# Optimization experiments

Hardware: AMD Instinct MI355X
Metric: run time of the kernel (lower is better)

Reference implementation:

```python
import jax, jax.numpy as jnp
import numpy as np

N, E = 50000, 800000
IN_C, HID, OUT_C = 128, 64, 40

def setup_inputs() -> dict:
    key = jax.random.key(0)
    ks = jax.random.split(key, 16)
    def w(k, shape, fan_in):
        return jax.random.normal(k, shape, dtype=jnp.float32) * (1.0 / np.sqrt(fan_in))
    x = jax.random.normal(ks[0], (N, IN_C), dtype=jnp.float32)
    edge_index = jax.random.randint(ks[1], (2, E), 0, N, dtype=jnp.int64)
    return {
        "x": x,
        "edge_index": edge_index,
        "W1": w(ks[2], (IN_C, HID), IN_C), "b1": jnp.zeros((HID,), jnp.float32),
        "W2": w(ks[3], (HID, HID), HID),   "b2": jnp.zeros((HID,), jnp.float32),
        "W3": w(ks[4], (HID, HID), HID),   "b3": jnp.zeros((HID,), jnp.float32),
        "g1": jnp.ones((HID,), jnp.float32), "be1": jnp.zeros((HID,), jnp.float32),
        "g2": jnp.ones((HID,), jnp.float32), "be2": jnp.zeros((HID,), jnp.float32),
        "M1": w(ks[5], (HID, HID), HID),   "mb1": jnp.zeros((HID,), jnp.float32),
        "M2": w(ks[6], (HID, OUT_C), HID), "mb2": jnp.zeros((OUT_C,), jnp.float32),
        "batch_size": N,
    }

def reference(x, edge_index, W1, b1, W2, b2, W3, b3, g1, be1, g2, be2, M1, mb1, M2, mb2, batch_size):
    src, dst = edge_index[0], edge_index[1]
    n = x.shape[0]
    # GCN symmetric norm with self-loops: deg over destination, +1 for self loop
    deg = jax.ops.segment_sum(jnp.ones(src.shape[0], x.dtype), dst, num_segments=n) + 1.0
    dinv = jax.lax.rsqrt(deg)  # deg >= 1 always
    enorm = (dinv[src] * dinv[dst])[:, None]  # [E,1]
    sloop = (dinv * dinv)[:, None]            # [N,1] self-loop norm

    def gcn_conv(h, W, b):
        hw = h @ W                                              # [N,H] transform first
        agg = jax.ops.segment_sum(enorm * hw[src], dst, num_segments=n)
        return agg + sloop * hw + b

    def layer_norm(h, g, be):
        mu = jnp.mean(h, axis=-1, keepdims=True)
        var = jnp.var(h, axis=-1, keepdims=True)
        return (h - mu) * jax.lax.rsqrt(var + 1e-5) * g + be

    h = jax.nn.relu(layer_norm(gcn_conv(x, W1, b1), g1, be1))
    h = jax.nn.relu(layer_norm(gcn_conv(h, W2, b2), g2, be2))
    h = gcn_conv(h, W3, b3)
    # MLP: Linear -> ReLU -> Linear
    h = jax.nn.relu(h @ M1 + mb1) @ M2 + mb2
    return jax.nn.softmax(h[:batch_size], axis=1)
```

## Files before the change

### kernel.cpp

```cpp
#include <hip/hip_runtime.h>
#include <hip/hip_fp16.h>
#include <math.h>

#define HID   64
#define OUTC  40
#define CAP   64

__global__ void zero_kernel(int4* __restrict__ p, int n4) {
    int i = blockIdx.x * blockDim.x + threadIdx.x;
    if (i < n4) p[i] = make_int4(0, 0, 0, 0);
}

__global__ void fill_kernel(const int* __restrict__ src, const int* __restrict__ dst,
                            int* __restrict__ cnt, unsigned short* __restrict__ recs,
                            int E, int N) {
    int g    = blockIdx.x & 7;
    int gblk = blockIdx.x >> 3;
    int nblk = gridDim.x >> 3;
    int slice = (N + 7) >> 3;
    int lo = g * slice;
    int hi = lo + slice; if (hi > N) hi = N;
    for (int e = gblk * blockDim.x + threadIdx.x; e < E; e += nblk * blockDim.x) {
        int d = dst[e];
        if (d >= lo && d < hi) {
            int pos = atomicAdd(&cnt[d], 1);
            if (pos < CAP) recs[(size_t)d * CAP + pos] = (unsigned short)src[e];
        }
    }
}

__global__ void dinv_kernel(const int* __restrict__ cnt, float* __restrict__ dinv, int N) {
    int i = blockIdx.x * blockDim.x + threadIdx.x;
    if (i < N) dinv[i] = rsqrtf((float)cnt[i] + 1.0f);
}

#define FMA16(acc, a, b) \
    acc[0][0] = fmaf(a.x, b.x, acc[0][0]); acc[0][1] = fmaf(a.x, b.y, acc[0][1]); \
    acc[0][2] = fmaf(a.x, b.z, acc[0][2]); acc[0][3] = fmaf(a.x, b.w, acc[0][3]); \
    acc[1][0] = fmaf(a.y, b.x, acc[1][0]); acc[1][1] = fmaf(a.y, b.y, acc[1][1]); \
    acc[1][2] = fmaf(a.y, b.z, acc[1][2]); acc[1][3] = fmaf(a.y, b.w, acc[1][3]); \
    acc[2][0] = fmaf(a.z, b.x, acc[2][0]); acc[2][1] = fmaf(a.z, b.y, acc[2][1]); \
    acc[2][2] = fmaf(a.z, b.z, acc[2][2]); acc[2][3] = fmaf(a.z, b.w, acc[2][3]); \
    acc[3][0] = fmaf(a.w, b.x, acc[3][0]); acc[3][1] = fmaf(a.w, b.y, acc[3][1]); \
    acc[3][2] = fmaf(a.w, b.z, acc[3][2]); acc[3][3] = fmaf(a.w, b.w, acc[3][3]);

template<int CIN, typename T>
__global__ __launch_bounds__(256) void xform_kernel(const T* __restrict__ X,
                                                    const float* __restrict__ W,
                                                    __half* __restrict__ out, int N) {
    __shared__ float Xs[CIN][68];
    __shared__ float Ws[CIN][68];
    int tid = threadIdx.x;
    int base = blockIdx.x << 6;
    int rows = N - base; if (rows > 64) rows = 64;

    {
        int k = tid >> 4, c = (tid & 15) << 2;
        #pragma unroll
        for (int k0 = 0; k0 < CIN; k0 += 16) {
            float4 wv = *(const float4*)(W + (size_t)((k0 + k) << 6) + c);
            *(float4*)&Ws[k0 + k][c] = wv;
        }
    }
    {
        int r = tid >> 2, q = (tid & 3) << 2;
        int rc = r < rows ? r : 0;
        const T* xp = X + (size_t)(base + rc) * CIN + q;
        #pragma unroll
        for (int k0 = 0; k0 < CIN; k0 += 16) {
            float4 xv;
            if constexpr (sizeof(T) == 4) {
                xv = *(const float4*)(xp + k0);
            } else {
                union { uint2 u; __half2 h[2]; } pk;
                pk.u = *(const uint2*)(xp + k0);
                float2 f01 = __half22float2(pk.h[0]);
                float2 f23 = __half22float2(pk.h[1]);
                xv = make_float4(f01.x, f01.y, f23.x, f23.y);
            }
            Xs[k0 + q + 0][r] = xv.x;
            Xs[k0 + q + 1][r] = xv.y;
            Xs[k0 + q + 2][r] = xv.z;
            Xs[k0 + q + 3][r] = xv.w;
        }
    }
    __syncthreads();

    int tx = tid & 15, ty = tid >> 4;
    float acc[4][4] = {};
    #pragma unroll 4
    for (int k = 0; k < CIN; k++) {
        float4 a = *(const float4*)&Xs[k][ty << 2];
        float4 b = *(const float4*)&Ws[k][tx << 2];
        FMA16(acc, a, b)
    }
    #pragma unroll
    for (int rr = 0; rr < 4; rr++) {
        int row = (ty << 2) + rr;
        if (row < rows) {
            union { uint2 u; __half2 h[2]; } pk;
            pk.h[0] = __float22half2_rn(make_float2(acc[rr][0], acc[rr][1]));
            pk.h[1] = __float22half2_rn(make_float2(acc[rr][2], acc[rr][3]));
            *(uint2*)(out + ((size_t)(base + row) << 6) + (tx << 2)) = pk.u;
        }
    }
}

template<bool LN>
__global__ void conv_kernel(const __half* __restrict__ hwh,
                            const unsigned short* __restrict__ recs,
                            const int* __restrict__ cnt, const float* __restrict__ dinv,
                            const float* __restrict__ b, const float* __restrict__ g,
                            const float* __restrict__ be, __half* __restrict__ out, int N) {
    int lane = threadIdx.x & 63;
    int row  = (blockIdx.x << 2) + (threadIdx.x >> 6);
    if (row >= N) return;

    int c = cnt[row]; if (c > CAP) c = CAP;
    int s_l = 0; float ds_l = 0.f;
    if (lane < c) { s_l = recs[(size_t)row * CAP + lane]; ds_l = dinv[s_l]; }

    int g8 = lane >> 3, j = lane & 7;
    const uint4* hw16 = (const uint4*)hwh;
    float di = dinv[row];
    uint4 selfv = hw16[(size_t)row * 8 + j];

    float acc[8] = {0,0,0,0,0,0,0,0};
    int kmax = (c + 15) & ~15;
    for (int k = 0; k < kmax; k += 16) {
        int   s0 = __shfl(s_l, k + g8),  s1 = __shfl(s_l, k + 8 + g8);
        float e0 = __shfl(ds_l, k + g8), e1 = __shfl(ds_l, k + 8 + g8);
        uint4 v0 = hw16[(size_t)s0 * 8 + j];
        uint4 v1 = hw16[(size_t)s1 * 8 + j];
        const __half2* h0 = (const __half2*)&v0;
        const __half2* h1 = (const __half2*)&v1;
        #pragma unroll
        for (int t = 0; t < 4; t++) {
            float2 f0 = __half22float2(h0[t]);
            float2 f1 = __half22float2(h1[t]);
            acc[2*t]   = fmaf(e0, f0.x, acc[2*t]);
            acc[2*t+1] = fmaf(e0, f0.y, acc[2*t+1]);
            acc[2*t]   = fmaf(e1, f1.x, acc[2*t]);
            acc[2*t+1] = fmaf(e1, f1.y, acc[2*t+1]);
        }
    }
    #pragma unroll
    for (int off = 8; off < 64; off <<= 1) {
        #pragma unroll
        for (int t = 0; t < 8; t++) acc[t] += __shfl_xor(acc[t], off);
    }

    int f0 = j << 3;
    const __half2* sp = (const __half2*)&selfv;
    float dd = di * di;
    float bb[8];
    *(float4*)&bb[0] = *(const float4*)(b + f0);
    *(float4*)&bb[4] = *(const float4*)(b + f0 + 4);
    #pragma unroll
    for (int t = 0; t < 4; t++) {
        float2 f = __half22float2(sp[t]);
        acc[2*t]   = fmaf(di, acc[2*t],   fmaf(dd, f.x, bb[2*t]));
        acc[2*t+1] = fmaf(di, acc[2*t+1], fmaf(dd, f.y, bb[2*t+1]));
    }

    if (LN) {
        float s = 0.f;
        #pragma unroll
        for (int t = 0; t < 8; t++) s += acc[t];
        #pragma unroll
        for (int o = 1; o < 8; o <<= 1) s += __shfl_xor(s, o);
        float mu = s * (1.f / 64.f);
        float v = 0.f;
        #pragma unroll
        for (int t = 0; t < 8; t++) { acc[t] -= mu; v += acc[t] * acc[t]; }
        #pragma unroll
        for (int o = 1; o < 8; o <<= 1) v += __shfl_xor(v, o);
        float r = rsqrtf(v * (1.f / 64.f) + 1e-5f);
        float gg[8], eb[8];
        *(float4*)&gg[0] = *(const float4*)(g + f0);
        *(float4*)&gg[4] = *(const float4*)(g + f0 + 4);
        *(float4*)&eb[0] = *(const float4*)(be + f0);
        *(float4*)&eb[4] = *(const float4*)(be + f0 + 4);
        #pragma unroll
        for (int t = 0; t < 8; t++)
            acc[t] = fmaxf(fmaf(acc[t] * r, gg[t], eb[t]), 0.f);
    }
    if (g8 == 0) {
        union { uint4 u; __half2 h[4]; } pk;
        #pragma unroll
        for (int t = 0; t < 4; t++)
            pk.h[t] = __float22half2_rn(make_float2(acc[2*t], acc[2*t+1]));
        *(uint4*)(out + (size_t)row * 64 + f0) = pk.u;
    }
}

__global__ __launch_bounds__(256) void mlp_kernel(const __half* __restrict__ h,
                           const float* __restrict__ M1, const float* __restrict__ mb1,
                           const float* __restrict__ M2, const float* __restrict__ mb2,
                           float* __restrict__ out, int N) {
    __shared__ float Hs [64][68];
    __shared__ float W1s[64][68];
    __shared__ float H2s[64][68];
    __shared__ float W2s[64][44];
    int tid = threadIdx.x;
    int base = blockIdx.x << 6;
    int rows = N - base; if (rows > 64) rows = 64;

    {
        int k = tid >> 4, c = (tid & 15) << 2;
        #pragma unroll
        for (int k0 = 0; k0 < 64; k0 += 16) {
            float4 wv = *(const float4*)(M1 + (size_t)((k0 + k) << 6) + c);
            *(float4*)&W1s[k0 + k][c] = wv;
        }
    }
    for (int i = tid; i < 64 * OUTC; i += 256)
        W2s[i / OUTC][i % OUTC] = M2[i];
    {
        int r = tid >> 2, q = (tid & 3) << 2;
        int rc = r < rows ? r : 0;
        const __half* xp = h + (((size_t)(base + rc)) << 6) + q;
        #pragma unroll
        for (int k0 = 0; k0 < 64; k0 += 16) {
            union { uint2 u; __half2 hh[2]; } pk;
            pk.u = *(const uint2*)(xp + k0);
            float2 f01 = __half22float2(pk.hh[0]);
            float2 f23 = __half22float2(pk.hh[1]);
            Hs[k0 + q + 0][r] = f01.x;
            Hs[k0 + q + 1][r] = f01.y;
            Hs[k0 + q + 2][r] = f23.x;
            Hs[k0 + q + 3][r] = f23.y;
        }
    }
    __syncthreads();

    int tx = tid & 15, ty = tid >> 4;

    float acc[4][4] = {};
    #pragma unroll 4
    for (int k = 0; k < 64; k++) {
        float4 a = *(const float4*)&Hs[k][ty << 2];
        float4 b = *(const float4*)&W1s[k][tx << 2];
        FMA16(acc, a, b)
    }
    float4 b1v = *(const float4*)(mb1 + (tx << 2));
    #pragma unroll
    for (int cc = 0; cc < 4; cc++) {
        float bc = cc == 0 ? b1v.x : cc == 1 ? b1v.y : cc == 2 ? b1v.z : b1v.w;
        #pragma unroll
        for (int rr = 0; rr < 4; rr++)
            H2s[(tx << 2) + cc][(ty << 2) + rr] = fmaxf(acc[rr][cc] + bc, 0.f);
    }
    __syncthreads();

    int bx = (tx < 10) ? (tx << 2) : 0;
    float acc2[4][4] = {};
    #pragma unroll 4
    for (int k = 0; k < 64; k++) {
        float4 a = *(const float4*)&H2s[k][ty << 2];
        float4 b = *(const float4*)&W2s[k][bx];
        FMA16(acc2, a, b)
    }
    float4 b2v = *(const float4*)(mb2 + bx);

    #pragma unroll
    for (int rr = 0; rr < 4; rr++) {
        float v0 = acc2[rr][0] + b2v.x, v1 = acc2[rr][1] + b2v.y;
        float v2 = acc2[rr][2] + b2v.z, v3 = acc2[rr][3] + b2v.w;
        float m = fmaxf(fmaxf(v0, v1), fmaxf(v2, v3));
        if (tx >= 10) m = -1e30f;
        #pragma unroll
        for (int s = 1; s < 16; s <<= 1) m = fmaxf(m, __shfl_xor(m, s));
        float e0 = __expf(v0 - m), e1 = __expf(v1 - m);
        float e2 = __expf(v2 - m), e3 = __expf(v3 - m);
        float sum = (tx < 10) ? (e0 + e1) + (e2 + e3) : 0.f;
        #pragma unroll
        for (int s = 1; s < 16; s <<= 1) sum += __shfl_xor(sum, s);
        float inv = 1.f / sum;
        int row = (ty << 2) + rr;
        if (tx < 10 && row < rows)
            *(float4*)(out + (size_t)(base + row) * OUTC + bx) =
                make_float4(e0 * inv, e1 * inv, e2 * inv, e3 * inv);
    }
}

extern "C" void kernel_launch(void* const* d_in, const int* in_sizes, int n_in,
                              void* d_out, int out_size, void* d_ws, size_t ws_size,
                              hipStream_t stream) {
    const float* x   = (const float*)d_in[0];
    const int*   ei  = (const int*)  d_in[1];
    const float* W1  = (const float*)d_in[2];
    const float* b1  = (const float*)d_in[3];
    const float* W2  = (const float*)d_in[4];
    const float* b2  = (const float*)d_in[5];
    const float* W3  = (const float*)d_in[6];
    const float* b3  = (const float*)d_in[7];
    const float* g1  = (const float*)d_in[8];
    const float* be1 = (const float*)d_in[9];
    const float* g2  = (const float*)d_in[10];
    const float* be2 = (const float*)d_in[11];
    const float* M1  = (const float*)d_in[12];
    const float* mb1 = (const float*)d_in[13];
    const float* M2  = (const float*)d_in[14];
    const float* mb2 = (const float*)d_in[15];

    const int IN_C = 128;
    int N = in_sizes[0] / IN_C;
    int E = in_sizes[1] / 2;
    const int* src = ei;
    const int* dst = ei + E;

    char* ws = (char*)d_ws;
    size_t off = 0;
    auto carve = [&](size_t bytes) -> void* {
        void* p = ws + off;
        off = (off + bytes + 255) & ~(size_t)255;
        return p;
    };
    int*            cnt  = (int*)           carve(((size_t)N + 4) * sizeof(int));
    float*          dinv = (float*)         carve((size_t)N * sizeof(float));
    unsigned short* recs = (unsigned short*)carve((size_t)N * CAP * sizeof(unsigned short));
    __half*         HWh  = (__half*)        carve((size_t)N * HID * sizeof(__half));
    __half*         H    = (__half*)        carve((size_t)N * HID * sizeof(__half));
    __half*         PH   = (__half*)        carve((size_t)N * HID * sizeof(__half));

    int n4 = (N + 3) / 4;
    zero_kernel<<<(n4 + 255) / 256, 256, 0, stream>>>((int4*)cnt, n4);

    int nb = (N + 255) / 256;
    int rb = (N + 3) / 4;
    int tb = (N + 63) / 64;

    fill_kernel<<<2048, 256, 0, stream>>>(src, dst, cnt, recs, E, N);
    dinv_kernel<<<nb, 256, 0, stream>>>(cnt, dinv, N);

    xform_kernel<128, float><<<tb, 256, 0, stream>>>(x, W1, HWh, N);
    conv_kernel<true><<<rb, 256, 0, stream>>>(HWh, recs, cnt, dinv, b1, g1, be1, H, N);
    xform_kernel<64, __half><<<tb, 256, 0, stream>>>(H, W2, HWh, N);
    conv_kernel<true><<<rb, 256, 0, stream>>>(HWh, recs, cnt, dinv, b2, g2, be2, H, N);
    xform_kernel<64, __half><<<tb, 256, 0, stream>>>(H, W3, HWh, N);
    conv_kernel<false><<<rb, 256, 0, stream>>>(HWh, recs, cnt, dinv, b3, nullptr, nullptr, PH, N);

    mlp_kernel<<<tb, 256, 0, stream>>>(PH, M1, mb1, M2, mb2, (float*)d_out, N);
}
```

Measured before the change: 187.5 us.

## Fold source-side GCN normalization into transform output and drop dinv kernel

The transform kernel now scales each output row by rsqrt(deg+1), so the aggregation kernel sums pre-normalized neighbor features and applies only the destination-side factor once. This removes the dinv kernel, the per-edge dinv gather and shuffles, and the per-edge multiplies. Padding lanes now point to a zeroed sentinel row N, which the transform kernel writes each launch and for which the buffers gain one extra row. Storing pre-scaled values in fp16 slightly changes rounding.

```diff
diff --git a/kernel.cpp b/kernel.cpp
--- a/kernel.cpp
+++ b/kernel.cpp
@@ -29,11 +29,6 @@
     }
 }
 
-__global__ void dinv_kernel(const int* __restrict__ cnt, float* __restrict__ dinv, int N) {
-    int i = blockIdx.x * blockDim.x + threadIdx.x;
-    if (i < N) dinv[i] = rsqrtf((float)cnt[i] + 1.0f);
-}
-
 #define FMA16(acc, a, b) \
     acc[0][0] = fmaf(a.x, b.x, acc[0][0]); acc[0][1] = fmaf(a.x, b.y, acc[0][1]); \
     acc[0][2] = fmaf(a.x, b.z, acc[0][2]); acc[0][3] = fmaf(a.x, b.w, acc[0][3]); \
@@ -47,6 +42,7 @@
 template<int CIN, typename T>
 __global__ __launch_bounds__(256) void xform_kernel(const T* __restrict__ X,
                                                     const float* __restrict__ W,
+                                                    const int* __restrict__ cnt,
                                                     __half* __restrict__ out, int N) {
     __shared__ float Xs[CIN][68];
     __shared__ float Ws[CIN][68];
@@ -98,38 +94,43 @@
     for (int rr = 0; rr < 4; rr++) {
         int row = (ty << 2) + rr;
         if (row < rows) {
+            float di = rsqrtf((float)cnt[base + row] + 1.0f);
             union { uint2 u; __half2 h[2]; } pk;
-            pk.h[0] = __float22half2_rn(make_float2(acc[rr][0], acc[rr][1]));
-            pk.h[1] = __float22half2_rn(make_float2(acc[rr][2], acc[rr][3]));
+            pk.h[0] = __float22half2_rn(make_float2(acc[rr][0] * di, acc[rr][1] * di));
+            pk.h[1] = __float22half2_rn(make_float2(acc[rr][2] * di, acc[rr][3] * di));
             *(uint2*)(out + ((size_t)(base + row) << 6) + (tx << 2)) = pk.u;
         }
+    }
+    if (blockIdx.x == gridDim.x - 1 && tid < 8) {
+        uint4 z = make_uint4(0, 0, 0, 0);
+        ((uint4*)(out + ((size_t)N << 6)))[tid] = z;
     }
 }
 
 template<bool LN>
 __global__ void conv_kernel(const __half* __restrict__ hwh,
                             const unsigned short* __restrict__ recs,
-                            const int* __restrict__ cnt, const float* __restrict__ dinv,
+                            const int* __restrict__ cnt,
                             const float* __restrict__ b, const float* __restrict__ g,
                             const float* __restrict__ be, __half* __restrict__ out, int N) {
     int lane = threadIdx.x & 63;
     int row  = (blockIdx.x << 2) + (threadIdx.x >> 6);
     if (row >= N) return;
 
-    int c = cnt[row]; if (c > CAP) c = CAP;
-    int s_l = 0; float ds_l = 0.f;
-    if (lane < c) { s_l = recs[(size_t)row * CAP + lane]; ds_l = dinv[s_l]; }
+    int cn = cnt[row];
+    int c  = cn > CAP ? CAP : cn;
+    int s_l = N;
+    if (lane < c) s_l = recs[(size_t)row * CAP + lane];
 
     int g8 = lane >> 3, j = lane & 7;
     const uint4* hw16 = (const uint4*)hwh;
-    float di = dinv[row];
+    float di = rsqrtf((float)cn + 1.0f);
     uint4 selfv = hw16[(size_t)row * 8 + j];
 
     float acc[8] = {0,0,0,0,0,0,0,0};
     int kmax = (c + 15) & ~15;
     for (int k = 0; k < kmax; k += 16) {
-        int   s0 = __shfl(s_l, k + g8),  s1 = __shfl(s_l, k + 8 + g8);
-        float e0 = __shfl(ds_l, k + g8), e1 = __shfl(ds_l, k + 8 + g8);
+        int s0 = __shfl(s_l, k + g8), s1 = __shfl(s_l, k + 8 + g8);
         uint4 v0 = hw16[(size_t)s0 * 8 + j];
         uint4 v1 = hw16[(size_t)s1 * 8 + j];
         const __half2* h0 = (const __half2*)&v0;
@@ -138,10 +139,8 @@
         for (int t = 0; t < 4; t++) {
             float2 f0 = __half22float2(h0[t]);
             float2 f1 = __half22float2(h1[t]);
-            acc[2*t]   = fmaf(e0, f0.x, acc[2*t]);
-            acc[2*t+1] = fmaf(e0, f0.y, acc[2*t+1]);
-            acc[2*t]   = fmaf(e1, f1.x, acc[2*t]);
-            acc[2*t+1] = fmaf(e1, f1.y, acc[2*t+1]);
+            acc[2*t]   += f0.x + f1.x;
+            acc[2*t+1] += f0.y + f1.y;
         }
     }
     #pragma unroll
@@ -152,15 +151,14 @@
 
     int f0 = j << 3;
     const __half2* sp = (const __half2*)&selfv;
-    float dd = di * di;
     float bb[8];
     *(float4*)&bb[0] = *(const float4*)(b + f0);
     *(float4*)&bb[4] = *(const float4*)(b + f0 + 4);
     #pragma unroll
     for (int t = 0; t < 4; t++) {
         float2 f = __half22float2(sp[t]);
-        acc[2*t]   = fmaf(di, acc[2*t],   fmaf(dd, f.x, bb[2*t]));
-        acc[2*t+1] = fmaf(di, acc[2*t+1], fmaf(dd, f.y, bb[2*t+1]));
+        acc[2*t]   = fmaf(di, acc[2*t]   + f.x, bb[2*t]);
+        acc[2*t+1] = fmaf(di, acc[2*t+1] + f.y, bb[2*t+1]);
     }
 
     if (LN) {
@@ -318,28 +316,25 @@
         return p;
     };
     int*            cnt  = (int*)           carve(((size_t)N + 4) * sizeof(int));
-    float*          dinv = (float*)         carve((size_t)N * sizeof(float));
     unsigned short* recs = (unsigned short*)carve((size_t)N * CAP * sizeof(unsigned short));
-    __half*         HWh  = (__half*)        carve((size_t)N * HID * sizeof(__half));
-    __half*         H    = (__half*)        carve((size_t)N * HID * sizeof(__half));
-    __half*         PH   = (__half*)        carve((size_t)N * HID * sizeof(__half));
+    __half*         HWh  = (__half*)        carve((size_t)(N + 1) * HID * sizeof(__half));
+    __half*         H    = (__half*)        carve((size_t)(N + 1) * HID * sizeof(__half));
+    __half*         PH   = (__half*)        carve((size_t)(N + 1) * HID * sizeof(__half));
 
     int n4 = (N + 3) / 4;
     zero_kernel<<<(n4 + 255) / 256, 256, 0, stream>>>((int4*)cnt, n4);
 
-    int nb = (N + 255) / 256;
     int rb = (N + 3) / 4;
     int tb = (N + 63) / 64;
 
     fill_kernel<<<2048, 256, 0, stream>>>(src, dst, cnt, recs, E, N);
-    dinv_kernel<<<nb, 256, 0, stream>>>(cnt, dinv, N);
-
-    xform_kernel<128, float><<<tb, 256, 0, stream>>>(x, W1, HWh, N);
-    conv_kernel<true><<<rb, 256, 0, stream>>>(HWh, recs, cnt, dinv, b1, g1, be1, H, N);
-    xform_kernel<64, __half><<<tb, 256, 0, stream>>>(H, W2, HWh, N);
-    conv_kernel<true><<<rb, 256, 0, stream>>>(HWh, recs, cnt, dinv, b2, g2, be2, H, N);
-    xform_kernel<64, __half><<<tb, 256, 0, stream>>>(H, W3, HWh, N);
-    conv_kernel<false><<<rb, 256, 0, stream>>>(HWh, recs, cnt, dinv, b3, nullptr, nullptr, PH, N);
+
+    xform_kernel<128, float><<<tb, 256, 0, stream>>>(x, W1, cnt, HWh, N);
+    conv_kernel<true><<<rb, 256, 0, stream>>>(HWh, recs, cnt, b1, g1, be1, H, N);
+    xform_kernel<64, __half><<<tb, 256, 0, stream>>>(H, W2, cnt, HWh, N);
+    conv_kernel<true><<<rb, 256, 0, stream>>>(HWh, recs, cnt, b2, g2, be2, H, N);
+    xform_kernel<64, __half><<<tb, 256, 0, stream>>>(H, W3, cnt, HWh, N);
+    conv_kernel<false><<<rb, 256, 0, stream>>>(HWh, recs, cnt, b3, nullptr, nullptr, PH, N);
 
     mlp_kernel<<<tb, 256, 0, stream>>>(PH, M1, mb1, M2, mb2, (float*)d_out, N);
 }
```

After: 186.8 us. Within noise of the previous version (-0.4%).
